# Performance work log

Hardware: AMD Instinct MI355X
Metric: run time of the kernel (lower is better)

The kernel has to match this reference:

```python
import jax, jax.numpy as jnp
import numpy as np

SOFTCLAMP = 50.0
CAUSAL_BLOCK = 256      # causal_block_size (tokens per time block)
NUM_SPECIAL = 8         # num_special_tokens
SPECIAL_SEQ = 2048      # block_size_per_special (defaults to kv seq len)
ROPE_BASE = 10000.0


def setup_inputs() -> dict:
    key = jax.random.key(0)
    kq, kk, kv = jax.random.split(key, 3)
    b, h, hk, s, d = 2, 16, 4, 2048, 64
    q = jax.random.normal(kq, (b, h, s, d), dtype=jnp.float32)
    k = jax.random.normal(kk, (b, hk, s, d), dtype=jnp.float32)
    v = jax.random.normal(kv, (b, hk, s, d), dtype=jnp.float32)
    # standard 1D rotary angles: [seq, dim_head]
    inv_freq = 1.0 / (ROPE_BASE ** (jnp.arange(0, d, 2, dtype=jnp.float32) / d))
    freqs = jnp.arange(s, dtype=jnp.float32)[:, None] * inv_freq[None, :]  # [s, d/2]
    rotations = jnp.concatenate((freqs, freqs), axis=-1)                   # [s, d]
    return {"q": q, "k": k, "v": v, "rotations": rotations}


def _apply_rotations(rotations, t):
    # t: [b, h, s, d]; rotations: [s, d] (broadcast over batch/heads)
    x1, x2 = jnp.split(t, 2, axis=-1)
    rotated_half = jnp.concatenate((-x2, x1), axis=-1)
    return t * jnp.cos(rotations) + rotated_half * jnp.sin(rotations)


def _forward(q, k, v, rotations):
    b, h, i, d = q.shape
    hk, j = k.shape[1], k.shape[2]
    scale = d ** -0.5
    q = _apply_rotations(rotations[:i], q)
    k = _apply_rotations(rotations[:j], k)
    g = h // hk  # GQA groups
    qg = q.reshape(b, hk, g, i, d)
    sim = jnp.einsum('bhgid,bhjd->bhgij', qg, k) * scale
    # softclamp score mod
    sim = jnp.tanh(sim / SOFTCLAMP) * SOFTCLAMP
    # special-token mask (faithful to source: compares raw q/k indices)
    qi = jnp.arange(i)[:, None]
    kj = jnp.arange(j)[None, :]
    special_start = SPECIAL_SEQ - NUM_SPECIAL
    q_is_special = qi >= special_start
    k_is_special = kj >= special_start
    special_mask = ~(~q_is_special & k_is_special)  # non-special q cannot see special k
    # block-causal mask: allowed when query block >= key block
    causal_allow = (qi // CAUSAL_BLOCK) >= (kj // CAUSAL_BLOCK)
    allow = special_mask & causal_allow  # [i, j], broadcasts over b,h,g
    mask_value = -jnp.finfo(sim.dtype).max
    sim = jnp.where(allow, sim, mask_value)
    attn = jax.nn.softmax(sim, axis=-1)
    out = jnp.einsum('bhgij,bhjd->bhgid', attn, v)
    return out.reshape(b, h, i, d)


def reference(q, k, v, rotations):
    return _forward(q, k, v, rotations)
```

## Files before the change

kernel.cpp:

```cpp
#include <hip/hip_runtime.h>
#include <stdint.h>

typedef unsigned short u16;
typedef short s16x8 __attribute__((ext_vector_type(8)));
typedef float f32x4 __attribute__((ext_vector_type(4)));

#define SQ 2048
#define DH 64
#define BM 128
#define BN 64
#define STR 72
#define SPECIAL_START 2040
#define NBH 32
#define NKV 8
#define NQP 16
#define NITEMS (NBH * NQP)
#define ATTN_GRID 448
#define K1F  0.18033688011112043f
#define KPAF 4.9244826e-9f
#define KPBF -6.406040185576019e-5f
#define KEF  36.067376022224085f

union U8 { s16x8 v; short e[8]; };
union F4 { f32x4 v; float e[4]; };

__device__ __forceinline__ u16 f2bf(float x) {
    uint32_t u = __float_as_uint(x);
    return (u16)((u + 0x7fffu + ((u >> 16) & 1u)) >> 16);
}
__device__ __forceinline__ uint32_t pkbf(float a, float b) {
    uint32_t r;
    asm("v_cvt_pk_bf16_f32 %0, %1, %2" : "=v"(r) : "v"(a), "v"(b));
    return r;
}
__device__ __forceinline__ float exp2hw(float x) {
    float r; asm("v_exp_f32 %0, %1" : "=v"(r) : "v"(x)); return r;
}
__device__ __forceinline__ float2 fsincos(float ang) {
    float r = ang * 0.15915494309189535f;
    r -= floorf(r);
    float s, c;
    asm("v_sin_f32 %0, %1" : "=v"(s) : "v"(r));
    asm("v_cos_f32 %0, %1" : "=v"(c) : "v"(r));
    return make_float2(s, c);
}

#define VTILES (NKV * 32)
#define RK (NKV * SQ)
#define KBLK (RK / 32)
__global__ __launch_bounds__(256)
void prep_kernel(const float* __restrict__ kg, const float* __restrict__ vg,
                 const float* __restrict__ rotg,
                 u16* __restrict__ kp, u16* __restrict__ vp,
                 uint32_t* __restrict__ cnt)
{
    const int tid = threadIdx.x;
    if (blockIdx.x == 0 && tid == 0) *cnt = 0u;
    if (blockIdx.x < VTILES) {
        __shared__ short Vls[64 * STR];
        const int tile = blockIdx.x;
        const float* src = vg + ((size_t)(tile >> 5) * SQ + (size_t)(tile & 31) * 64) * DH;
        {
            int kv = tid >> 2, c0 = (tid & 3) * 16;
            const float* s4 = src + (size_t)kv * DH + c0;
            float4 f0 = *(const float4*)(s4);
            float4 f1 = *(const float4*)(s4 + 4);
            float4 f2 = *(const float4*)(s4 + 8);
            float4 f3 = *(const float4*)(s4 + 12);
            uint4 w0 = make_uint4(pkbf(f0.x, f0.y), pkbf(f0.z, f0.w),
                                  pkbf(f1.x, f1.y), pkbf(f1.z, f1.w));
            uint4 w1 = make_uint4(pkbf(f2.x, f2.y), pkbf(f2.z, f2.w),
                                  pkbf(f3.x, f3.y), pkbf(f3.z, f3.w));
            *(uint4*)&Vls[kv * STR + c0]     = w0;
            *(uint4*)&Vls[kv * STR + c0 + 8] = w1;
        }
        __syncthreads();
        {
            int d = tid >> 2, c0 = (tid & 3) * 16;
            U8 o0, o1;
#pragma unroll
            for (int j = 0; j < 16; j++)
                (j < 8 ? o0 : o1).e[j & 7] = Vls[(c0 + j) * STR + d];
            u16* dst = vp + (((size_t)tile * 64 + d) << 6) + c0;
            *(s16x8*)dst       = o0.v;
            *(s16x8*)(dst + 8) = o1.v;
        }
    } else {
        int bx = blockIdx.x - VTILES;
        int r8 = tid >> 3, c0 = (tid & 7) * 4;
        int r = bx * 32 + r8;
        const int s = r & (SQ - 1);
        const float* src = kg + (size_t)r * DH;
        u16*         dst = kp + (size_t)r * DH;
        float4 a  = *(const float4*)(src + c0);
        float4 b  = *(const float4*)(src + c0 + 32);
        float4 rv = *(const float4*)(rotg + (size_t)s * DH + c0);
        float2 s0 = fsincos(rv.x), s1 = fsincos(rv.y),
               s2 = fsincos(rv.z), s3 = fsincos(rv.w);
        float lo0 = a.x * s0.y - b.x * s0.x, hi0 = b.x * s0.y + a.x * s0.x;
        float lo1 = a.y * s1.y - b.y * s1.x, hi1 = b.y * s1.y + a.y * s1.x;
        float lo2 = a.z * s2.y - b.z * s2.x, hi2 = b.z * s2.y + a.z * s2.x;
        float lo3 = a.w * s3.y - b.w * s3.x, hi3 = b.w * s3.y + a.w * s3.x;
        *(uint2*)(dst + c0)      = make_uint2(pkbf(lo0, lo1), pkbf(lo2, lo3));
        *(uint2*)(dst + c0 + 32) = make_uint2(pkbf(hi0, hi1), pkbf(hi2, hi3));
    }
}

__global__ __launch_bounds__(256, 3)
void attn_fast(const float* __restrict__ qg, const float* __restrict__ rotg,
               const u16* __restrict__ kp, const u16* __restrict__ vp,
               uint32_t* __restrict__ cnt, float* __restrict__ outg)
{
    const int tid = threadIdx.x;
    const int wv = tid >> 6, lane = tid & 63;
    const int l15 = lane & 15, quad = lane >> 4;
    const int swl = (l15 & 7) << 3;
    const int r4 = tid >> 2, c16 = (tid & 3) * 16;
    const int swr = (r4 & 7) << 3;

    __shared__ __align__(16) short Ks[2][BN * 64];
    __shared__ __align__(16) short Vt[2][DH * 64];
    __shared__ __align__(16) short Ps[BM * 64];
    __shared__ int s_w;

    for (;;) {
        __syncthreads();
        if (tid == 0) s_w = (int)atomicAdd(cnt, 1u);
        __syncthreads();
        const int w = s_w;
        if (w >= NITEMS) break;
        const int qp = (NQP - 1) - (w >> 5);
        const int u  = w & 31, bkv = u >> 2;
        const int bh = ((bkv >> 2) << 4) | ((bkv & 3) << 2) | (u & 3);
        const int nkt = ((qp >> 1) + 1) << 2;
        const int qrow0 = qp * BM + wv * 32;

        s16x8 qf[2][2];
#pragma unroll
        for (int nq = 0; nq < 2; nq++) {
            const int srow = qrow0 + nq * 16 + l15;
            const float* gq = qg + ((size_t)bh * SQ + srow) * DH + quad * 8;
            float a[8], b[8];
            *(float4*)&a[0] = *(const float4*)(gq);
            *(float4*)&a[4] = *(const float4*)(gq + 4);
            *(float4*)&b[0] = *(const float4*)(gq + 32);
            *(float4*)&b[4] = *(const float4*)(gq + 36);
            const float* rrow = rotg + (size_t)srow * DH + quad * 8;
            float lo[8], hi[8];
#pragma unroll
            for (int j = 0; j < 8; j++) {
                float2 sc = fsincos(rrow[j]);
                lo[j] = a[j] * sc.y - b[j] * sc.x;
                hi[j] = b[j] * sc.y + a[j] * sc.x;
            }
            U8 q0, q1;
#pragma unroll
            for (int j = 0; j < 4; j++) {
                ((uint32_t*)&q0.v)[j] = pkbf(lo[2 * j], lo[2 * j + 1]);
                ((uint32_t*)&q1.v)[j] = pkbf(hi[2 * j], hi[2 * j + 1]);
            }
            qf[nq][0] = q0.v;
            qf[nq][1] = q1.v;
        }

        const u16* kbase = kp + (size_t)bkv * (SQ * DH);
        const u16* vbase = vp + (size_t)bkv * (32 * 64 * 64);
        s16x8 kpr0, kpr1, vpr0, vpr1;
        auto pref = [&](int kt) {
            const u16* srck = kbase + (size_t)(kt * BN + r4) * DH + c16;
            kpr0 = *(const s16x8*)srck;
            kpr1 = *(const s16x8*)(srck + 8);
            const u16* srcv = vbase + ((size_t)kt << 12) + (r4 << 6) + c16;
            vpr0 = *(const s16x8*)srcv;
            vpr1 = *(const s16x8*)(srcv + 8);
        };
        pref(0);

        F4 oa[2][4];
#pragma unroll
        for (int nq = 0; nq < 2; nq++)
#pragma unroll
            for (int mb = 0; mb < 4; mb++) oa[nq][mb].v = (f32x4){0.f, 0.f, 0.f, 0.f};
        float lsum0 = 0.f, lsum1 = 0.f;
        short* prow0 = &Ps[(wv * 32 + l15) * 64];
        short* prow1 = &Ps[(wv * 32 + 16 + l15) * 64];

#pragma unroll 2
        for (int kt = 0; kt < nkt; kt++) {
            const int cb = kt & 1;
            *(s16x8*)&Ks[cb][r4 * 64 + (c16 ^ swr)]        = kpr0;
            *(s16x8*)&Ks[cb][r4 * 64 + ((c16 + 8) ^ swr)]  = kpr1;
            *(s16x8*)&Vt[cb][r4 * 64 + (c16 ^ swr)]        = vpr0;
            *(s16x8*)&Vt[cb][r4 * 64 + ((c16 + 8) ^ swr)]  = vpr1;
            if (kt + 1 < nkt) pref(kt + 1);
            __syncthreads();

            F4 sa[2][4];
            __builtin_amdgcn_s_setprio(1);
#pragma unroll
            for (int ks = 0; ks < 2; ks++)
#pragma unroll
                for (int mb = 0; mb < 4; mb++) {
                    s16x8 kf = *(const s16x8*)&Ks[cb][(mb * 16 + l15) * 64 + ((ks * 32 + quad * 8) ^ swl)];
                    sa[0][mb].v = __builtin_amdgcn_mfma_f32_16x16x32_bf16(
                        kf, qf[0][ks], ks ? sa[0][mb].v : (f32x4){0.f, 0.f, 0.f, 0.f}, 0, 0, 0);
                    sa[1][mb].v = __builtin_amdgcn_mfma_f32_16x16x32_bf16(
                        kf, qf[1][ks], ks ? sa[1][mb].v : (f32x4){0.f, 0.f, 0.f, 0.f}, 0, 0, 0);
                }
            __builtin_amdgcn_s_setprio(0);

            const int last = (kt == 31);
#pragma unroll
            for (int nq = 0; nq < 2; nq++) {
                const int qglob = qrow0 + nq * 16 + l15;
                short* prow = nq ? prow1 : prow0;
                float ls = 0.f;
#pragma unroll
                for (int mb = 0; mb < 4; mb++) {
                    F4 pa;
#pragma unroll
                    for (int c = 0; c < 4; c++) {
                        float t  = sa[nq][mb].e[c] * K1F;
                        float w2 = t * t;
                        float poly = fmaf(w2, fmaf(w2, KPAF, KPBF), 1.0f);
                        pa.e[c] = exp2hw(fmaf(t, poly, -KEF));
                    }
                    if (last && qglob < SPECIAL_START) {
#pragma unroll
                        for (int c = 0; c < 4; c++) {
                            int kvglob = kt * BN + mb * 16 + quad * 4 + c;
                            if (kvglob >= SPECIAL_START) pa.e[c] = 0.f;
                        }
                    }
                    ls += (pa.e[0] + pa.e[1]) + (pa.e[2] + pa.e[3]);
                    uint2 pw = make_uint2(pkbf(pa.e[0], pa.e[1]),
                                          pkbf(pa.e[2], pa.e[3]));
                    *(uint2*)&prow[(mb * 16 + quad * 4) ^ swl] = pw;
                }
                if (nq) lsum1 += ls; else lsum0 += ls;
            }

            __builtin_amdgcn_s_setprio(1);
#pragma unroll
            for (int ks = 0; ks < 2; ks++) {
                s16x8 pf0 = *(const s16x8*)&prow0[(ks * 32 + quad * 8) ^ swl];
                s16x8 pf1 = *(const s16x8*)&prow1[(ks * 32 + quad * 8) ^ swl];
#pragma unroll
                for (int mb = 0; mb < 4; mb++) {
                    s16x8 vf = *(const s16x8*)&Vt[cb][(mb * 16 + l15) * 64 + ((ks * 32 + quad * 8) ^ swl)];
                    oa[0][mb].v = __builtin_amdgcn_mfma_f32_16x16x32_bf16(vf, pf0, oa[0][mb].v, 0, 0, 0);
                    oa[1][mb].v = __builtin_amdgcn_mfma_f32_16x16x32_bf16(vf, pf1, oa[1][mb].v, 0, 0, 0);
                }
            }
            __builtin_amdgcn_s_setprio(0);
        }

        lsum0 += __shfl_xor(lsum0, 16, 64);
        lsum0 += __shfl_xor(lsum0, 32, 64);
        lsum1 += __shfl_xor(lsum1, 16, 64);
        lsum1 += __shfl_xor(lsum1, 32, 64);

#pragma unroll
        for (int nq = 0; nq < 2; nq++) {
            float rl = 1.0f / (nq ? lsum1 : lsum0);
            int qrow = qrow0 + nq * 16 + l15;
            float* orow = outg + ((size_t)bh * SQ + qrow) * DH;
#pragma unroll
            for (int mb = 0; mb < 4; mb++) {
                int d0 = mb * 16 + quad * 4;
                *(float4*)(orow + d0) = make_float4(oa[nq][mb].e[0] * rl, oa[nq][mb].e[1] * rl,
                                                    oa[nq][mb].e[2] * rl, oa[nq][mb].e[3] * rl);
            }
        }
    }
}

__global__ __launch_bounds__(256, 4)
void attn_fallback(const float* __restrict__ qg, const float* __restrict__ kg,
                   const float* __restrict__ vg, const float* __restrict__ rotg,
                   float* __restrict__ outg)
{
    const int x  = blockIdx.x;
    const int qt = (x & 1) ? (31 - (x >> 1)) : (x >> 1);
    const int bh = blockIdx.y;
    const int bb = bh >> 4, hh = bh & 15;
    const int bkv = bb * 4 + (hh >> 2);
    const int qs = qt * 64;

    const int tid = threadIdx.x;
    const int wv = tid >> 6, lane = tid & 63;
    const int l15 = lane & 15, quad = lane >> 4;
    const int swl = (l15 & 7) << 3;

    __shared__ __align__(16) short QPs[64 * 64];
    __shared__ __align__(16) short Ks[2][BN * 64];
    __shared__ __align__(16) short Vt[2][DH * 64];

    const size_t kvbase = ((size_t)bkv * SQ) * DH;
    const int nkt = (qt / 4 + 1) * 4;
    const int qglob = qs + wv * 16 + l15;

    {
        int rr = tid >> 2, c0 = (tid & 3) * 8;
        int srow = qs + rr;
        const float* gq = qg + ((size_t)bh * SQ + srow) * DH;
        float a[8], b[8];
        *(float4*)&a[0] = *(const float4*)(gq + c0);
        *(float4*)&a[4] = *(const float4*)(gq + c0 + 4);
        *(float4*)&b[0] = *(const float4*)(gq + c0 + 32);
        *(float4*)&b[4] = *(const float4*)(gq + c0 + 36);
        U8 o0, o1;
#pragma unroll
        for (int j = 0; j < 8; j++) {
            float2 sc = fsincos(rotg[(size_t)srow * DH + c0 + j]);
            o0.e[j] = (short)f2bf(a[j] * sc.y - b[j] * sc.x);
            o1.e[j] = (short)f2bf(b[j] * sc.y + a[j] * sc.x);
        }
        int sw2 = (rr & 7) << 3;
        *(s16x8*)&QPs[rr * 64 + (c0 ^ sw2)]        = o0.v;
        *(s16x8*)&QPs[rr * 64 + ((c0 + 32) ^ sw2)] = o1.v;
    }
    __syncthreads();

    s16x8 qf[2];
#pragma unroll
    for (int ks = 0; ks < 2; ks++)
        qf[ks] = *(const s16x8*)&QPs[(wv * 16 + l15) * 64 + ((ks * 32 + quad * 8) ^ swl)];

    F4 oa[4];
#pragma unroll
    for (int mb = 0; mb < 4; mb++) oa[mb].v = (f32x4){0.f, 0.f, 0.f, 0.f};
    float lsum = 0.f;

    for (int kt = 0; kt < nkt; kt++) {
        const int cb = kt & 1;
        {
            int rr = tid >> 2, c0 = (tid & 3) * 8;
            int srow = kt * BN + rr;
            const float* gk = kg + kvbase + (size_t)srow * DH;
            float a[8], b[8];
            *(float4*)&a[0] = *(const float4*)(gk + c0);
            *(float4*)&a[4] = *(const float4*)(gk + c0 + 4);
            *(float4*)&b[0] = *(const float4*)(gk + c0 + 32);
            *(float4*)&b[4] = *(const float4*)(gk + c0 + 36);
            U8 o0, o1;
#pragma unroll
            for (int j = 0; j < 8; j++) {
                float2 sc = fsincos(rotg[(size_t)(srow & (SQ - 1)) * DH + c0 + j]);
                o0.e[j] = (short)f2bf(a[j] * sc.y - b[j] * sc.x);
                o1.e[j] = (short)f2bf(b[j] * sc.y + a[j] * sc.x);
            }
            int sw2 = (rr & 7) << 3;
            *(s16x8*)&Ks[cb][rr * 64 + (c0 ^ sw2)]        = o0.v;
            *(s16x8*)&Ks[cb][rr * 64 + ((c0 + 32) ^ sw2)] = o1.v;
        }
        {
            int rr = tid >> 2, c0 = (tid & 3) * 16;
            const float* gv = vg + kvbase + (size_t)(kt * BN + rr) * DH;
            float vv[16];
#pragma unroll
            for (int t = 0; t < 4; t++)
                *(float4*)&vv[t * 4] = *(const float4*)(gv + c0 + t * 4);
#pragma unroll
            for (int j = 0; j < 16; j++) {
                int d = c0 + j;
                Vt[cb][d * 64 + (rr ^ ((d & 7) << 3))] = (short)f2bf(vv[j]);
            }
        }
        __syncthreads();

        F4 sa[4];
#pragma unroll
        for (int mb = 0; mb < 4; mb++) sa[mb].v = (f32x4){0.f, 0.f, 0.f, 0.f};
#pragma unroll
        for (int ks = 0; ks < 2; ks++)
#pragma unroll
            for (int mb = 0; mb < 4; mb++) {
                s16x8 kf = *(const s16x8*)&Ks[cb][(mb * 16 + l15) * 64 + ((ks * 32 + quad * 8) ^ swl)];
                sa[mb].v = __builtin_amdgcn_mfma_f32_16x16x32_bf16(kf, qf[ks], sa[mb].v, 0, 0, 0);
            }

        F4 pa[4];
#pragma unroll
        for (int mb = 0; mb < 4; mb++)
#pragma unroll
            for (int c = 0; c < 4; c++) {
                float t  = sa[mb].e[c] * K1F;
                float w2 = t * t;
                float poly = fmaf(w2, fmaf(w2, KPAF, KPBF), 1.0f);
                pa[mb].e[c] = exp2hw(fmaf(t, poly, -KEF));
            }
        if (kt == 31 && qglob < SPECIAL_START) {
#pragma unroll
            for (int mb = 0; mb < 4; mb++)
#pragma unroll
                for (int c = 0; c < 4; c++) {
                    int kvglob = kt * BN + mb * 16 + quad * 4 + c;
                    if (kvglob >= SPECIAL_START) pa[mb].e[c] = 0.f;
                }
        }
        short* prow = &QPs[(wv * 16 + l15) * 64];
#pragma unroll
        for (int mb = 0; mb < 4; mb++) {
            lsum += (pa[mb].e[0] + pa[mb].e[1]) + (pa[mb].e[2] + pa[mb].e[3]);
            uint2 pw = make_uint2(pkbf(pa[mb].e[0], pa[mb].e[1]),
                                  pkbf(pa[mb].e[2], pa[mb].e[3]));
            *(uint2*)&prow[(mb * 16 + quad * 4) ^ swl] = pw;
        }
#pragma unroll
        for (int ks = 0; ks < 2; ks++) {
            s16x8 pf = *(const s16x8*)&prow[(ks * 32 + quad * 8) ^ swl];
#pragma unroll
            for (int mb = 0; mb < 4; mb++) {
                s16x8 vf = *(const s16x8*)&Vt[cb][(mb * 16 + l15) * 64 + ((ks * 32 + quad * 8) ^ swl)];
                oa[mb].v = __builtin_amdgcn_mfma_f32_16x16x32_bf16(vf, pf, oa[mb].v, 0, 0, 0);
            }
        }
        __syncthreads();
    }

    lsum += __shfl_xor(lsum, 16, 64);
    lsum += __shfl_xor(lsum, 32, 64);

    float rl = 1.0f / lsum;
    int qrow = qs + wv * 16 + l15;
    float* orow = outg + ((size_t)bh * SQ + qrow) * DH;
#pragma unroll
    for (int mb = 0; mb < 4; mb++) {
        int d0 = mb * 16 + quad * 4;
        *(float4*)(orow + d0) = make_float4(oa[mb].e[0] * rl, oa[mb].e[1] * rl,
                                            oa[mb].e[2] * rl, oa[mb].e[3] * rl);
    }
}

extern "C" void kernel_launch(void* const* d_in, const int* in_sizes, int n_in,
                              void* d_out, int out_size, void* d_ws, size_t ws_size,
                              hipStream_t stream) {
    const float* q   = (const float*)d_in[0];
    const float* k   = (const float*)d_in[1];
    const float* v   = (const float*)d_in[2];
    const float* rot = (const float*)d_in[3];
    float* out = (float*)d_out;

    char* w = (char*)d_ws;
    const size_t k_bytes = (size_t)NKV * SQ * DH * sizeof(u16);
    const size_t v_bytes = k_bytes;
    u16* kp = (u16*)w;
    u16* vp = (u16*)(w + k_bytes);
    uint32_t* cnt = (uint32_t*)(w + k_bytes + v_bytes);

    if (ws_size >= k_bytes + v_bytes + sizeof(uint32_t)) {
        hipLaunchKernelGGL(prep_kernel, dim3(VTILES + KBLK), dim3(256), 0, stream,
                           k, v, rot, kp, vp, cnt);
        hipLaunchKernelGGL(attn_fast, dim3(ATTN_GRID), dim3(256), 0, stream,
                           q, rot, kp, vp, cnt, out);
    } else {
        hipLaunchKernelGGL(attn_fallback, dim3(32, NBH), dim3(256), 0, stream,
                           q, k, v, rot, out);
    }
}
```

Measured before the change: 135.8 us.

## Split each query tile's KV range across two wave groups per block

The attention block grows to 512 threads, split into two groups of four waves. Each group processes half of the query tile's key/value tiles using its own LDS staging. The second group writes its partial output and row sums to shared memory, and the first group adds them in before normalising and storing. The goal is to halve per-work-item latency and cut tail imbalance from causal work skew in the persistent scheduler. In exchange, K/V double buffering is dropped, an extra barrier is added per tile, a combine step is added, and the grid size changes.

```diff
diff --git a/kernel.cpp b/kernel.cpp
--- a/kernel.cpp
+++ b/kernel.cpp
@@ -15,7 +15,7 @@
 #define NKV 8
 #define NQP 16
 #define NITEMS (NBH * NQP)
-#define ATTN_GRID 448
+#define ATTN_GRID 480
 #define K1F  0.18033688011112043f
 #define KPAF 4.9244826e-9f
 #define KPBF -6.406040185576019e-5f
@@ -106,7 +106,7 @@
     }
 }
 
-__global__ __launch_bounds__(256, 3)
+__global__ __launch_bounds__(512, 4)
 void attn_fast(const float* __restrict__ qg, const float* __restrict__ rotg,
                const u16* __restrict__ kp, const u16* __restrict__ vp,
                uint32_t* __restrict__ cnt, float* __restrict__ outg)
@@ -114,14 +114,19 @@
     const int tid = threadIdx.x;
     const int wv = tid >> 6, lane = tid & 63;
     const int l15 = lane & 15, quad = lane >> 4;
+    const int grp = wv >> 2, wl = wv & 3;
+    const int tl = tid & 255;
+    const int r4 = tl >> 2, c16 = (tl & 3) * 16;
+    const int swr = (r4 & 7) << 3;
     const int swl = (l15 & 7) << 3;
-    const int r4 = tid >> 2, c16 = (tid & 3) * 16;
-    const int swr = (r4 & 7) << 3;
-
-    __shared__ __align__(16) short Ks[2][BN * 64];
-    __shared__ __align__(16) short Vt[2][DH * 64];
-    __shared__ __align__(16) short Ps[BM * 64];
+
+    __shared__ __align__(16) short SM[32768];
     __shared__ int s_w;
+    short* Ksg  = SM + grp * 4096;
+    short* Vtg  = SM + 8192 + grp * 4096;
+    short* Psg  = SM + 16384 + grp * 8192;
+    float* comb  = (float*)SM;
+    float* lsumB = (float*)(SM + 16384);
 
     for (;;) {
         __syncthreads();
@@ -133,35 +138,9 @@
         const int u  = w & 31, bkv = u >> 2;
         const int bh = ((bkv >> 2) << 4) | ((bkv & 3) << 2) | (u & 3);
         const int nkt = ((qp >> 1) + 1) << 2;
-        const int qrow0 = qp * BM + wv * 32;
-
-        s16x8 qf[2][2];
-#pragma unroll
-        for (int nq = 0; nq < 2; nq++) {
-            const int srow = qrow0 + nq * 16 + l15;
-            const float* gq = qg + ((size_t)bh * SQ + srow) * DH + quad * 8;
-            float a[8], b[8];
-            *(float4*)&a[0] = *(const float4*)(gq);
-            *(float4*)&a[4] = *(const float4*)(gq + 4);
-            *(float4*)&b[0] = *(const float4*)(gq + 32);
-            *(float4*)&b[4] = *(const float4*)(gq + 36);
-            const float* rrow = rotg + (size_t)srow * DH + quad * 8;
-            float lo[8], hi[8];
-#pragma unroll
-            for (int j = 0; j < 8; j++) {
-                float2 sc = fsincos(rrow[j]);
-                lo[j] = a[j] * sc.y - b[j] * sc.x;
-                hi[j] = b[j] * sc.y + a[j] * sc.x;
-            }
-            U8 q0, q1;
-#pragma unroll
-            for (int j = 0; j < 4; j++) {
-                ((uint32_t*)&q0.v)[j] = pkbf(lo[2 * j], lo[2 * j + 1]);
-                ((uint32_t*)&q1.v)[j] = pkbf(hi[2 * j], hi[2 * j + 1]);
-            }
-            qf[nq][0] = q0.v;
-            qf[nq][1] = q1.v;
-        }
+        const int h   = nkt >> 1;
+        const int kt0 = grp ? h : 0;
+        const int qrow0 = qp * BM + wl * 32;
 
         const u16* kbase = kp + (size_t)bkv * (SQ * DH);
         const u16* vbase = vp + (size_t)bkv * (32 * 64 * 64);
@@ -174,7 +153,35 @@
             vpr0 = *(const s16x8*)srcv;
             vpr1 = *(const s16x8*)(srcv + 8);
         };
-        pref(0);
+        pref(kt0);
+
+        s16x8 qf[2][2];
+#pragma unroll
+        for (int nq = 0; nq < 2; nq++) {
+            const int srow = qrow0 + nq * 16 + l15;
+            const float* gq = qg + ((size_t)bh * SQ + srow) * DH + quad * 8;
+            float a[8], b[8];
+            *(float4*)&a[0] = *(const float4*)(gq);
+            *(float4*)&a[4] = *(const float4*)(gq + 4);
+            *(float4*)&b[0] = *(const float4*)(gq + 32);
+            *(float4*)&b[4] = *(const float4*)(gq + 36);
+            const float* rrow = rotg + (size_t)srow * DH + quad * 8;
+            float lo[8], hi[8];
+#pragma unroll
+            for (int j = 0; j < 8; j++) {
+                float2 sc = fsincos(rrow[j]);
+                lo[j] = a[j] * sc.y - b[j] * sc.x;
+                hi[j] = b[j] * sc.y + a[j] * sc.x;
+            }
+            U8 q0, q1;
+#pragma unroll
+            for (int j = 0; j < 4; j++) {
+                ((uint32_t*)&q0.v)[j] = pkbf(lo[2 * j], lo[2 * j + 1]);
+                ((uint32_t*)&q1.v)[j] = pkbf(hi[2 * j], hi[2 * j + 1]);
+            }
+            qf[nq][0] = q0.v;
+            qf[nq][1] = q1.v;
+        }
 
         F4 oa[2][4];
 #pragma unroll
@@ -182,17 +189,16 @@
 #pragma unroll
             for (int mb = 0; mb < 4; mb++) oa[nq][mb].v = (f32x4){0.f, 0.f, 0.f, 0.f};
         float lsum0 = 0.f, lsum1 = 0.f;
-        short* prow0 = &Ps[(wv * 32 + l15) * 64];
-        short* prow1 = &Ps[(wv * 32 + 16 + l15) * 64];
-
-#pragma unroll 2
-        for (int kt = 0; kt < nkt; kt++) {
-            const int cb = kt & 1;
-            *(s16x8*)&Ks[cb][r4 * 64 + (c16 ^ swr)]        = kpr0;
-            *(s16x8*)&Ks[cb][r4 * 64 + ((c16 + 8) ^ swr)]  = kpr1;
-            *(s16x8*)&Vt[cb][r4 * 64 + (c16 ^ swr)]        = vpr0;
-            *(s16x8*)&Vt[cb][r4 * 64 + ((c16 + 8) ^ swr)]  = vpr1;
-            if (kt + 1 < nkt) pref(kt + 1);
+        short* prow0 = &Psg[(wl * 32 + l15) * 64];
+        short* prow1 = &Psg[(wl * 32 + 16 + l15) * 64];
+
+        for (int i = 0; i < h; i++) {
+            const int kt = kt0 + i;
+            *(s16x8*)&Ksg[r4 * 64 + (c16 ^ swr)]       = kpr0;
+            *(s16x8*)&Ksg[r4 * 64 + ((c16 + 8) ^ swr)] = kpr1;
+            *(s16x8*)&Vtg[r4 * 64 + (c16 ^ swr)]       = vpr0;
+            *(s16x8*)&Vtg[r4 * 64 + ((c16 + 8) ^ swr)] = vpr1;
+            if (i + 1 < h) pref(kt + 1);
             __syncthreads();
 
             F4 sa[2][4];
@@ -201,7 +207,7 @@
             for (int ks = 0; ks < 2; ks++)
 #pragma unroll
                 for (int mb = 0; mb < 4; mb++) {
-                    s16x8 kf = *(const s16x8*)&Ks[cb][(mb * 16 + l15) * 64 + ((ks * 32 + quad * 8) ^ swl)];
+                    s16x8 kf = *(const s16x8*)&Ksg[(mb * 16 + l15) * 64 + ((ks * 32 + quad * 8) ^ swl)];
                     sa[0][mb].v = __builtin_amdgcn_mfma_f32_16x16x32_bf16(
                         kf, qf[0][ks], ks ? sa[0][mb].v : (f32x4){0.f, 0.f, 0.f, 0.f}, 0, 0, 0);
                     sa[1][mb].v = __builtin_amdgcn_mfma_f32_16x16x32_bf16(
@@ -247,12 +253,13 @@
                 s16x8 pf1 = *(const s16x8*)&prow1[(ks * 32 + quad * 8) ^ swl];
 #pragma unroll
                 for (int mb = 0; mb < 4; mb++) {
-                    s16x8 vf = *(const s16x8*)&Vt[cb][(mb * 16 + l15) * 64 + ((ks * 32 + quad * 8) ^ swl)];
+                    s16x8 vf = *(const s16x8*)&Vtg[(mb * 16 + l15) * 64 + ((ks * 32 + quad * 8) ^ swl)];
                     oa[0][mb].v = __builtin_amdgcn_mfma_f32_16x16x32_bf16(vf, pf0, oa[0][mb].v, 0, 0, 0);
                     oa[1][mb].v = __builtin_amdgcn_mfma_f32_16x16x32_bf16(vf, pf1, oa[1][mb].v, 0, 0, 0);
                 }
             }
             __builtin_amdgcn_s_setprio(0);
+            __syncthreads();
         }
 
         lsum0 += __shfl_xor(lsum0, 16, 64);
@@ -260,16 +267,34 @@
         lsum1 += __shfl_xor(lsum1, 16, 64);
         lsum1 += __shfl_xor(lsum1, 32, 64);
 
-#pragma unroll
-        for (int nq = 0; nq < 2; nq++) {
-            float rl = 1.0f / (nq ? lsum1 : lsum0);
-            int qrow = qrow0 + nq * 16 + l15;
-            float* orow = outg + ((size_t)bh * SQ + qrow) * DH;
-#pragma unroll
-            for (int mb = 0; mb < 4; mb++) {
-                int d0 = mb * 16 + quad * 4;
-                *(float4*)(orow + d0) = make_float4(oa[nq][mb].e[0] * rl, oa[nq][mb].e[1] * rl,
-                                                    oa[nq][mb].e[2] * rl, oa[nq][mb].e[3] * rl);
+        if (grp) {
+#pragma unroll
+            for (int nq = 0; nq < 2; nq++) {
+                const int row = wl * 32 + nq * 16 + l15;
+#pragma unroll
+                for (int mb = 0; mb < 4; mb++)
+                    *(float4*)&comb[row * 64 + mb * 16 + quad * 4] =
+                        make_float4(oa[nq][mb].e[0], oa[nq][mb].e[1],
+                                    oa[nq][mb].e[2], oa[nq][mb].e[3]);
+                if (quad == 0) lsumB[row] = nq ? lsum1 : lsum0;
+            }
+        }
+        __syncthreads();
+        if (!grp) {
+#pragma unroll
+            for (int nq = 0; nq < 2; nq++) {
+                const int row = wl * 32 + nq * 16 + l15;
+                const float rl = 1.0f / ((nq ? lsum1 : lsum0) + lsumB[row]);
+                float* orow = outg + ((size_t)bh * SQ + qp * BM + row) * DH;
+#pragma unroll
+                for (int mb = 0; mb < 4; mb++) {
+                    const int d0 = mb * 16 + quad * 4;
+                    float4 cb = *(float4*)&comb[row * 64 + d0];
+                    *(float4*)(orow + d0) = make_float4((oa[nq][mb].e[0] + cb.x) * rl,
+                                                        (oa[nq][mb].e[1] + cb.y) * rl,
+                                                        (oa[nq][mb].e[2] + cb.z) * rl,
+                                                        (oa[nq][mb].e[3] + cb.w) * rl);
+                }
             }
         }
     }
@@ -452,7 +477,7 @@
     if (ws_size >= k_bytes + v_bytes + sizeof(uint32_t)) {
         hipLaunchKernelGGL(prep_kernel, dim3(VTILES + KBLK), dim3(256), 0, stream,
                            k, v, rot, kp, vp, cnt);
-        hipLaunchKernelGGL(attn_fast, dim3(ATTN_GRID), dim3(256), 0, stream,
+        hipLaunchKernelGGL(attn_fast, dim3(ATTN_GRID), dim3(512), 0, stream,
                            q, rot, kp, vp, cnt, out);
     } else {
         hipLaunchKernelGGL(attn_fallback, dim3(32, NBH), dim3(256), 0, stream,
```

New measurement: 135.7 us. About the same (-0.1%).

## Make attention waves independent, loading K/V fragments directly from global memory

Applied to the files above, without the earlier changes.

Each wave now takes its own 32-row query work item from the atomic queue instead of a 4-wave block sharing one 128-row tile. The shared-memory staging of K and V and the block barriers are removed, and each wave loads MFMA fragments for K and V straight from global memory, prefetching the next tile after each MFMA phase. The P buffer becomes per-wave with padded stride, the row sums accumulate as vectors, and the grid grows to 768 blocks. The cost is no K/V reuse across the waves of a block, so global and L2 traffic rises, plus more atomics.

```diff
diff --git a/kernel.cpp b/kernel.cpp
--- a/kernel.cpp
+++ b/kernel.cpp
@@ -7,15 +7,14 @@
 
 #define SQ 2048
 #define DH 64
-#define BM 128
 #define BN 64
 #define STR 72
+#define PSTR 72
 #define SPECIAL_START 2040
 #define NBH 32
 #define NKV 8
-#define NQP 16
-#define NITEMS (NBH * NQP)
-#define ATTN_GRID 448
+#define NITEMS 2048
+#define ATTN_BLOCKS 768
 #define K1F  0.18033688011112043f
 #define KPAF 4.9244826e-9f
 #define KPBF -6.406040185576019e-5f
@@ -106,39 +105,58 @@
     }
 }
 
-__global__ __launch_bounds__(256, 3)
+__global__ __launch_bounds__(256)
+__attribute__((amdgpu_waves_per_eu(3, 3)))
 void attn_fast(const float* __restrict__ qg, const float* __restrict__ rotg,
                const u16* __restrict__ kp, const u16* __restrict__ vp,
                uint32_t* __restrict__ cnt, float* __restrict__ outg)
 {
-    const int tid = threadIdx.x;
-    const int wv = tid >> 6, lane = tid & 63;
+    const int lane = threadIdx.x & 63;
+    const int wv   = threadIdx.x >> 6;
     const int l15 = lane & 15, quad = lane >> 4;
-    const int swl = (l15 & 7) << 3;
-    const int r4 = tid >> 2, c16 = (tid & 3) * 16;
-    const int swr = (r4 & 7) << 3;
-
-    __shared__ __align__(16) short Ks[2][BN * 64];
-    __shared__ __align__(16) short Vt[2][DH * 64];
-    __shared__ __align__(16) short Ps[BM * 64];
-    __shared__ int s_w;
+
+    __shared__ __align__(16) short Ps[4][32 * PSTR];
+    short* prow0 = &Ps[wv][l15 * PSTR];
+    short* prow1 = &Ps[wv][(16 + l15) * PSTR];
 
     for (;;) {
-        __syncthreads();
-        if (tid == 0) s_w = (int)atomicAdd(cnt, 1u);
-        __syncthreads();
-        const int w = s_w;
+        int w = 0;
+        if (lane == 0) w = (int)atomicAdd(cnt, 1u);
+        w = __shfl(w, 0, 64);
         if (w >= NITEMS) break;
-        const int qp = (NQP - 1) - (w >> 5);
-        const int u  = w & 31, bkv = u >> 2;
-        const int bh = ((bkv >> 2) << 4) | ((bkv & 3) << 2) | (u & 3);
-        const int nkt = ((qp >> 1) + 1) << 2;
-        const int qrow0 = qp * BM + wv * 32;
+        const int idx = 63 - (w >> 5);
+        const int u   = w & 31, bkv = u >> 2;
+        const int bh  = ((bkv >> 2) << 4) | ((bkv & 3) << 2) | (u & 3);
+        const int qs  = idx * 32;
+        const int nkt = ((idx >> 3) + 1) << 2;
+
+        const u16* kptr = kp + (size_t)bkv * (SQ * DH) + l15 * DH + quad * 8;
+        const u16* vptr = vp + (size_t)bkv * (SQ * DH) + l15 * DH + quad * 8;
+
+        s16x8 kf0[4], kf1[4], vf0[4], vf1[4];
+        auto loadK = [&](int kt) {
+            const u16* p = kptr + ((size_t)kt << 12);
+#pragma unroll
+            for (int mb = 0; mb < 4; mb++) {
+                kf0[mb] = *(const s16x8*)(p + mb * 1024);
+                kf1[mb] = *(const s16x8*)(p + mb * 1024 + 32);
+            }
+        };
+        auto loadV = [&](int kt) {
+            const u16* p = vptr + ((size_t)kt << 12);
+#pragma unroll
+            for (int mb = 0; mb < 4; mb++) {
+                vf0[mb] = *(const s16x8*)(p + mb * 1024);
+                vf1[mb] = *(const s16x8*)(p + mb * 1024 + 32);
+            }
+        };
+        loadK(0);
+        loadV(0);
 
         s16x8 qf[2][2];
 #pragma unroll
         for (int nq = 0; nq < 2; nq++) {
-            const int srow = qrow0 + nq * 16 + l15;
+            const int srow = qs + nq * 16 + l15;
             const float* gq = qg + ((size_t)bh * SQ + srow) * DH + quad * 8;
             float a[8], b[8];
             *(float4*)&a[0] = *(const float4*)(gq);
@@ -163,68 +181,52 @@
             qf[nq][1] = q1.v;
         }
 
-        const u16* kbase = kp + (size_t)bkv * (SQ * DH);
-        const u16* vbase = vp + (size_t)bkv * (32 * 64 * 64);
-        s16x8 kpr0, kpr1, vpr0, vpr1;
-        auto pref = [&](int kt) {
-            const u16* srck = kbase + (size_t)(kt * BN + r4) * DH + c16;
-            kpr0 = *(const s16x8*)srck;
-            kpr1 = *(const s16x8*)(srck + 8);
-            const u16* srcv = vbase + ((size_t)kt << 12) + (r4 << 6) + c16;
-            vpr0 = *(const s16x8*)srcv;
-            vpr1 = *(const s16x8*)(srcv + 8);
-        };
-        pref(0);
-
-        F4 oa[2][4];
-#pragma unroll
-        for (int nq = 0; nq < 2; nq++)
-#pragma unroll
-            for (int mb = 0; mb < 4; mb++) oa[nq][mb].v = (f32x4){0.f, 0.f, 0.f, 0.f};
-        float lsum0 = 0.f, lsum1 = 0.f;
-        short* prow0 = &Ps[(wv * 32 + l15) * 64];
-        short* prow1 = &Ps[(wv * 32 + 16 + l15) * 64];
-
-#pragma unroll 2
+        F4 oa0[4], oa1[4], lsa0, lsa1;
+#pragma unroll
+        for (int mb = 0; mb < 4; mb++) {
+            oa0[mb].v = (f32x4){0.f, 0.f, 0.f, 0.f};
+            oa1[mb].v = (f32x4){0.f, 0.f, 0.f, 0.f};
+        }
+        lsa0.v = (f32x4){0.f, 0.f, 0.f, 0.f};
+        lsa1.v = (f32x4){0.f, 0.f, 0.f, 0.f};
+
         for (int kt = 0; kt < nkt; kt++) {
-            const int cb = kt & 1;
-            *(s16x8*)&Ks[cb][r4 * 64 + (c16 ^ swr)]        = kpr0;
-            *(s16x8*)&Ks[cb][r4 * 64 + ((c16 + 8) ^ swr)]  = kpr1;
-            *(s16x8*)&Vt[cb][r4 * 64 + (c16 ^ swr)]        = vpr0;
-            *(s16x8*)&Vt[cb][r4 * 64 + ((c16 + 8) ^ swr)]  = vpr1;
-            if (kt + 1 < nkt) pref(kt + 1);
-            __syncthreads();
-
-            F4 sa[2][4];
+            F4 sa0[4], sa1[4];
             __builtin_amdgcn_s_setprio(1);
 #pragma unroll
-            for (int ks = 0; ks < 2; ks++)
+            for (int mb = 0; mb < 4; mb++) {
+                sa0[mb].v = __builtin_amdgcn_mfma_f32_16x16x32_bf16(
+                    kf0[mb], qf[0][0], (f32x4){0.f, 0.f, 0.f, 0.f}, 0, 0, 0);
+                sa1[mb].v = __builtin_amdgcn_mfma_f32_16x16x32_bf16(
+                    kf0[mb], qf[1][0], (f32x4){0.f, 0.f, 0.f, 0.f}, 0, 0, 0);
+            }
+#pragma unroll
+            for (int mb = 0; mb < 4; mb++) {
+                sa0[mb].v = __builtin_amdgcn_mfma_f32_16x16x32_bf16(
+                    kf1[mb], qf[0][1], sa0[mb].v, 0, 0, 0);
+                sa1[mb].v = __builtin_amdgcn_mfma_f32_16x16x32_bf16(
+                    kf1[mb], qf[1][1], sa1[mb].v, 0, 0, 0);
+            }
+            __builtin_amdgcn_s_setprio(0);
+            if (kt + 1 < nkt) loadK(kt + 1);
+
+            const int last = (kt == 31);
+#pragma unroll
+            for (int nq = 0; nq < 2; nq++) {
+                const int qglob = qs + nq * 16 + l15;
+                short* prow = nq ? prow1 : prow0;
 #pragma unroll
                 for (int mb = 0; mb < 4; mb++) {
-                    s16x8 kf = *(const s16x8*)&Ks[cb][(mb * 16 + l15) * 64 + ((ks * 32 + quad * 8) ^ swl)];
-                    sa[0][mb].v = __builtin_amdgcn_mfma_f32_16x16x32_bf16(
-                        kf, qf[0][ks], ks ? sa[0][mb].v : (f32x4){0.f, 0.f, 0.f, 0.f}, 0, 0, 0);
-                    sa[1][mb].v = __builtin_amdgcn_mfma_f32_16x16x32_bf16(
-                        kf, qf[1][ks], ks ? sa[1][mb].v : (f32x4){0.f, 0.f, 0.f, 0.f}, 0, 0, 0);
-                }
-            __builtin_amdgcn_s_setprio(0);
-
-            const int last = (kt == 31);
-#pragma unroll
-            for (int nq = 0; nq < 2; nq++) {
-                const int qglob = qrow0 + nq * 16 + l15;
-                short* prow = nq ? prow1 : prow0;
-                float ls = 0.f;
-#pragma unroll
-                for (int mb = 0; mb < 4; mb++) {
-                    F4 pa;
-#pragma unroll
-                    for (int c = 0; c < 4; c++) {
-                        float t  = sa[nq][mb].e[c] * K1F;
-                        float w2 = t * t;
-                        float poly = fmaf(w2, fmaf(w2, KPAF, KPBF), 1.0f);
-                        pa.e[c] = exp2hw(fmaf(t, poly, -KEF));
-                    }
+                    F4 t, w2, py, pa;
+                    t.v  = (nq ? sa1[mb].v : sa0[mb].v) * K1F;
+                    w2.v = t.v * t.v;
+                    py.v = w2.v * KPAF + KPBF;
+                    py.v = w2.v * py.v + 1.0f;
+                    t.v  = t.v * py.v - KEF;
+                    pa.e[0] = exp2hw(t.e[0]);
+                    pa.e[1] = exp2hw(t.e[1]);
+                    pa.e[2] = exp2hw(t.e[2]);
+                    pa.e[3] = exp2hw(t.e[3]);
                     if (last && qglob < SPECIAL_START) {
 #pragma unroll
                         for (int c = 0; c < 4; c++) {
@@ -232,29 +234,34 @@
                             if (kvglob >= SPECIAL_START) pa.e[c] = 0.f;
                         }
                     }
-                    ls += (pa.e[0] + pa.e[1]) + (pa.e[2] + pa.e[3]);
+                    if (nq) lsa1.v = lsa1.v + pa.v; else lsa0.v = lsa0.v + pa.v;
                     uint2 pw = make_uint2(pkbf(pa.e[0], pa.e[1]),
                                           pkbf(pa.e[2], pa.e[3]));
-                    *(uint2*)&prow[(mb * 16 + quad * 4) ^ swl] = pw;
+                    *(uint2*)&prow[mb * 16 + quad * 4] = pw;
                 }
-                if (nq) lsum1 += ls; else lsum0 += ls;
-            }
-
+            }
+
+            s16x8 pf00 = *(const s16x8*)&prow0[quad * 8];
+            s16x8 pf01 = *(const s16x8*)&prow0[32 + quad * 8];
+            s16x8 pf10 = *(const s16x8*)&prow1[quad * 8];
+            s16x8 pf11 = *(const s16x8*)&prow1[32 + quad * 8];
             __builtin_amdgcn_s_setprio(1);
 #pragma unroll
-            for (int ks = 0; ks < 2; ks++) {
-                s16x8 pf0 = *(const s16x8*)&prow0[(ks * 32 + quad * 8) ^ swl];
-                s16x8 pf1 = *(const s16x8*)&prow1[(ks * 32 + quad * 8) ^ swl];
-#pragma unroll
-                for (int mb = 0; mb < 4; mb++) {
-                    s16x8 vf = *(const s16x8*)&Vt[cb][(mb * 16 + l15) * 64 + ((ks * 32 + quad * 8) ^ swl)];
-                    oa[0][mb].v = __builtin_amdgcn_mfma_f32_16x16x32_bf16(vf, pf0, oa[0][mb].v, 0, 0, 0);
-                    oa[1][mb].v = __builtin_amdgcn_mfma_f32_16x16x32_bf16(vf, pf1, oa[1][mb].v, 0, 0, 0);
-                }
+            for (int mb = 0; mb < 4; mb++) {
+                oa0[mb].v = __builtin_amdgcn_mfma_f32_16x16x32_bf16(vf0[mb], pf00, oa0[mb].v, 0, 0, 0);
+                oa1[mb].v = __builtin_amdgcn_mfma_f32_16x16x32_bf16(vf0[mb], pf10, oa1[mb].v, 0, 0, 0);
+            }
+#pragma unroll
+            for (int mb = 0; mb < 4; mb++) {
+                oa0[mb].v = __builtin_amdgcn_mfma_f32_16x16x32_bf16(vf1[mb], pf01, oa0[mb].v, 0, 0, 0);
+                oa1[mb].v = __builtin_amdgcn_mfma_f32_16x16x32_bf16(vf1[mb], pf11, oa1[mb].v, 0, 0, 0);
             }
             __builtin_amdgcn_s_setprio(0);
-        }
-
+            if (kt + 1 < nkt) loadV(kt + 1);
+        }
+
+        float lsum0 = (lsa0.e[0] + lsa0.e[1]) + (lsa0.e[2] + lsa0.e[3]);
+        float lsum1 = (lsa1.e[0] + lsa1.e[1]) + (lsa1.e[2] + lsa1.e[3]);
         lsum0 += __shfl_xor(lsum0, 16, 64);
         lsum0 += __shfl_xor(lsum0, 32, 64);
         lsum1 += __shfl_xor(lsum1, 16, 64);
@@ -262,14 +269,15 @@
 
 #pragma unroll
         for (int nq = 0; nq < 2; nq++) {
-            float rl = 1.0f / (nq ? lsum1 : lsum0);
-            int qrow = qrow0 + nq * 16 + l15;
+            const float rl = 1.0f / (nq ? lsum1 : lsum0);
+            const int qrow = qs + nq * 16 + l15;
             float* orow = outg + ((size_t)bh * SQ + qrow) * DH;
 #pragma unroll
             for (int mb = 0; mb < 4; mb++) {
-                int d0 = mb * 16 + quad * 4;
-                *(float4*)(orow + d0) = make_float4(oa[nq][mb].e[0] * rl, oa[nq][mb].e[1] * rl,
-                                                    oa[nq][mb].e[2] * rl, oa[nq][mb].e[3] * rl);
+                const int d0 = mb * 16 + quad * 4;
+                const F4& o = nq ? oa1[mb] : oa0[mb];
+                *(float4*)(orow + d0) = make_float4(o.e[0] * rl, o.e[1] * rl,
+                                                    o.e[2] * rl, o.e[3] * rl);
             }
         }
     }
@@ -452,7 +460,7 @@
     if (ws_size >= k_bytes + v_bytes + sizeof(uint32_t)) {
         hipLaunchKernelGGL(prep_kernel, dim3(VTILES + KBLK), dim3(256), 0, stream,
                            k, v, rot, kp, vp, cnt);
-        hipLaunchKernelGGL(attn_fast, dim3(ATTN_GRID), dim3(256), 0, stream,
+        hipLaunchKernelGGL(attn_fast, dim3(ATTN_BLOCKS), dim3(256), 0, stream,
                            q, rot, kp, vp, cnt, out);
     } else {
         hipLaunchKernelGGL(attn_fallback, dim3(32, NBH), dim3(256), 0, stream,
```

Measured after the change: 215.1 us. 1.58x slower.

## Stage K/V tiles with direct global-to-LDS loads and restructure the pipeline

Applied to the files above, without the earlier changes.

K and V tiles now go straight from global memory into LDS through global_load_lds, replacing the register prefetch and the explicit LDS stores. The barrier moves to the end of each iteration, and the swizzle is folded into the global read offsets. The grid size and occupancy hints change, the exp polynomial is vectorized, and the row sums are kept as vector accumulators. The aim is to cut VGPR pressure and LDS store instructions, at the risk of a synchronization hazard if the async LDS writes are not fully waited on before use.

```diff
diff --git a/kernel.cpp b/kernel.cpp
--- a/kernel.cpp
+++ b/kernel.cpp
@@ -7,7 +7,6 @@
 
 #define SQ 2048
 #define DH 64
-#define BM 128
 #define BN 64
 #define STR 72
 #define SPECIAL_START 2040
@@ -15,7 +14,7 @@
 #define NKV 8
 #define NQP 16
 #define NITEMS (NBH * NQP)
-#define ATTN_GRID 448
+#define ATTN_GRID 512
 #define K1F  0.18033688011112043f
 #define KPAF 4.9244826e-9f
 #define KPBF -6.406040185576019e-5f
@@ -43,6 +42,11 @@
     asm("v_sin_f32 %0, %1" : "=v"(s) : "v"(r));
     asm("v_cos_f32 %0, %1" : "=v"(c) : "v"(r));
     return make_float2(s, c);
+}
+__device__ __forceinline__ void gl_lds16(const void* g, void* l) {
+    __builtin_amdgcn_global_load_lds(
+        (const __attribute__((address_space(1))) uint32_t*)g,
+        (__attribute__((address_space(3))) uint32_t*)l, 16, 0, 0);
 }
 
 #define VTILES (NKV * 32)
@@ -106,7 +110,8 @@
     }
 }
 
-__global__ __launch_bounds__(256, 3)
+__global__ __launch_bounds__(256)
+__attribute__((amdgpu_waves_per_eu(3, 4)))
 void attn_fast(const float* __restrict__ qg, const float* __restrict__ rotg,
                const u16* __restrict__ kp, const u16* __restrict__ vp,
                uint32_t* __restrict__ cnt, float* __restrict__ outg)
@@ -115,13 +120,20 @@
     const int wv = tid >> 6, lane = tid & 63;
     const int l15 = lane & 15, quad = lane >> 4;
     const int swl = (l15 & 7) << 3;
-    const int r4 = tid >> 2, c16 = (tid & 3) * 16;
-    const int swr = (r4 & 7) << 3;
-
-    __shared__ __align__(16) short Ks[2][BN * 64];
-    __shared__ __align__(16) short Vt[2][DH * 64];
-    __shared__ __align__(16) short Ps[BM * 64];
+
+    __shared__ __align__(16) u16 Ks[2][4096];
+    __shared__ __align__(16) u16 Vt[2][4096];
+    __shared__ __align__(16) short Ps[128 * 64];
     __shared__ int s_w;
+
+    const int gcol = (((lane & 7) ^ (lane >> 3)) << 3);
+    const int goff0 = ((wv * 16 + (lane >> 3)) << 6) + gcol;
+    const int goff1 = goff0 + (8 << 6);
+    const int lds0 = (wv * 2) * 512;
+    const int lds1 = lds0 + 512;
+
+    short* prow0 = &Ps[(wv * 32 + l15) * 64];
+    short* prow1 = &Ps[(wv * 32 + 16 + l15) * 64];
 
     for (;;) {
         __syncthreads();
@@ -132,8 +144,20 @@
         const int qp = (NQP - 1) - (w >> 5);
         const int u  = w & 31, bkv = u >> 2;
         const int bh = ((bkv >> 2) << 4) | ((bkv & 3) << 2) | (u & 3);
-        const int nkt = ((qp >> 1) + 1) << 2;
-        const int qrow0 = qp * BM + wv * 32;
+        const int nkt = (((qp >> 1) + 1)) << 2;
+        const int qrow0 = qp * 128 + wv * 32;
+
+        const u16* kbase = kp + (size_t)bkv * (SQ * DH);
+        const u16* vbase = vp + (size_t)bkv * (SQ * DH);
+        auto stage = [&](int kt, int cb) {
+            const u16* tk = kbase + ((size_t)kt << 12);
+            const u16* tv = vbase + ((size_t)kt << 12);
+            gl_lds16(tk + goff0, &Ks[cb][lds0]);
+            gl_lds16(tk + goff1, &Ks[cb][lds1]);
+            gl_lds16(tv + goff0, &Vt[cb][lds0]);
+            gl_lds16(tv + goff1, &Vt[cb][lds1]);
+        };
+        stage(0, 0);
 
         s16x8 qf[2][2];
 #pragma unroll
@@ -163,37 +187,20 @@
             qf[nq][1] = q1.v;
         }
 
-        const u16* kbase = kp + (size_t)bkv * (SQ * DH);
-        const u16* vbase = vp + (size_t)bkv * (32 * 64 * 64);
-        s16x8 kpr0, kpr1, vpr0, vpr1;
-        auto pref = [&](int kt) {
-            const u16* srck = kbase + (size_t)(kt * BN + r4) * DH + c16;
-            kpr0 = *(const s16x8*)srck;
-            kpr1 = *(const s16x8*)(srck + 8);
-            const u16* srcv = vbase + ((size_t)kt << 12) + (r4 << 6) + c16;
-            vpr0 = *(const s16x8*)srcv;
-            vpr1 = *(const s16x8*)(srcv + 8);
-        };
-        pref(0);
-
         F4 oa[2][4];
 #pragma unroll
         for (int nq = 0; nq < 2; nq++)
 #pragma unroll
             for (int mb = 0; mb < 4; mb++) oa[nq][mb].v = (f32x4){0.f, 0.f, 0.f, 0.f};
-        float lsum0 = 0.f, lsum1 = 0.f;
-        short* prow0 = &Ps[(wv * 32 + l15) * 64];
-        short* prow1 = &Ps[(wv * 32 + 16 + l15) * 64];
-
-#pragma unroll 2
+        F4 lsa0, lsa1;
+        lsa0.v = (f32x4){0.f, 0.f, 0.f, 0.f};
+        lsa1.v = (f32x4){0.f, 0.f, 0.f, 0.f};
+
+        __syncthreads();
+        int cb = 0;
+
         for (int kt = 0; kt < nkt; kt++) {
-            const int cb = kt & 1;
-            *(s16x8*)&Ks[cb][r4 * 64 + (c16 ^ swr)]        = kpr0;
-            *(s16x8*)&Ks[cb][r4 * 64 + ((c16 + 8) ^ swr)]  = kpr1;
-            *(s16x8*)&Vt[cb][r4 * 64 + (c16 ^ swr)]        = vpr0;
-            *(s16x8*)&Vt[cb][r4 * 64 + ((c16 + 8) ^ swr)]  = vpr1;
-            if (kt + 1 < nkt) pref(kt + 1);
-            __syncthreads();
+            if (kt + 1 < nkt) stage(kt + 1, cb ^ 1);
 
             F4 sa[2][4];
             __builtin_amdgcn_s_setprio(1);
@@ -214,17 +221,18 @@
             for (int nq = 0; nq < 2; nq++) {
                 const int qglob = qrow0 + nq * 16 + l15;
                 short* prow = nq ? prow1 : prow0;
-                float ls = 0.f;
 #pragma unroll
                 for (int mb = 0; mb < 4; mb++) {
-                    F4 pa;
-#pragma unroll
-                    for (int c = 0; c < 4; c++) {
-                        float t  = sa[nq][mb].e[c] * K1F;
-                        float w2 = t * t;
-                        float poly = fmaf(w2, fmaf(w2, KPAF, KPBF), 1.0f);
-                        pa.e[c] = exp2hw(fmaf(t, poly, -KEF));
-                    }
+                    F4 t, w2, py, pa;
+                    t.v  = sa[nq][mb].v * K1F;
+                    w2.v = t.v * t.v;
+                    py.v = w2.v * KPAF + KPBF;
+                    py.v = w2.v * py.v + 1.0f;
+                    t.v  = t.v * py.v - KEF;
+                    pa.e[0] = exp2hw(t.e[0]);
+                    pa.e[1] = exp2hw(t.e[1]);
+                    pa.e[2] = exp2hw(t.e[2]);
+                    pa.e[3] = exp2hw(t.e[3]);
                     if (last && qglob < SPECIAL_START) {
 #pragma unroll
                         for (int c = 0; c < 4; c++) {
@@ -232,29 +240,38 @@
                             if (kvglob >= SPECIAL_START) pa.e[c] = 0.f;
                         }
                     }
-                    ls += (pa.e[0] + pa.e[1]) + (pa.e[2] + pa.e[3]);
+                    if (nq) lsa1.v = lsa1.v + pa.v; else lsa0.v = lsa0.v + pa.v;
                     uint2 pw = make_uint2(pkbf(pa.e[0], pa.e[1]),
                                           pkbf(pa.e[2], pa.e[3]));
                     *(uint2*)&prow[(mb * 16 + quad * 4) ^ swl] = pw;
                 }
-                if (nq) lsum1 += ls; else lsum0 += ls;
-            }
-
+            }
+
+            s16x8 pf00 = *(const s16x8*)&prow0[(quad * 8) ^ swl];
+            s16x8 pf01 = *(const s16x8*)&prow0[(32 + quad * 8) ^ swl];
+            s16x8 pf10 = *(const s16x8*)&prow1[(quad * 8) ^ swl];
+            s16x8 pf11 = *(const s16x8*)&prow1[(32 + quad * 8) ^ swl];
             __builtin_amdgcn_s_setprio(1);
 #pragma unroll
-            for (int ks = 0; ks < 2; ks++) {
-                s16x8 pf0 = *(const s16x8*)&prow0[(ks * 32 + quad * 8) ^ swl];
-                s16x8 pf1 = *(const s16x8*)&prow1[(ks * 32 + quad * 8) ^ swl];
-#pragma unroll
-                for (int mb = 0; mb < 4; mb++) {
-                    s16x8 vf = *(const s16x8*)&Vt[cb][(mb * 16 + l15) * 64 + ((ks * 32 + quad * 8) ^ swl)];
-                    oa[0][mb].v = __builtin_amdgcn_mfma_f32_16x16x32_bf16(vf, pf0, oa[0][mb].v, 0, 0, 0);
-                    oa[1][mb].v = __builtin_amdgcn_mfma_f32_16x16x32_bf16(vf, pf1, oa[1][mb].v, 0, 0, 0);
-                }
+            for (int mb = 0; mb < 4; mb++) {
+                s16x8 vf = *(const s16x8*)&Vt[cb][(mb * 16 + l15) * 64 + ((quad * 8) ^ swl)];
+                oa[0][mb].v = __builtin_amdgcn_mfma_f32_16x16x32_bf16(vf, pf00, oa[0][mb].v, 0, 0, 0);
+                oa[1][mb].v = __builtin_amdgcn_mfma_f32_16x16x32_bf16(vf, pf10, oa[1][mb].v, 0, 0, 0);
+            }
+#pragma unroll
+            for (int mb = 0; mb < 4; mb++) {
+                s16x8 vf = *(const s16x8*)&Vt[cb][(mb * 16 + l15) * 64 + ((32 + quad * 8) ^ swl)];
+                oa[0][mb].v = __builtin_amdgcn_mfma_f32_16x16x32_bf16(vf, pf01, oa[0][mb].v, 0, 0, 0);
+                oa[1][mb].v = __builtin_amdgcn_mfma_f32_16x16x32_bf16(vf, pf11, oa[1][mb].v, 0, 0, 0);
             }
             __builtin_amdgcn_s_setprio(0);
-        }
-
+
+            __syncthreads();
+            cb ^= 1;
+        }
+
+        float lsum0 = (lsa0.e[0] + lsa0.e[1]) + (lsa0.e[2] + lsa0.e[3]);
+        float lsum1 = (lsa1.e[0] + lsa1.e[1]) + (lsa1.e[2] + lsa1.e[3]);
         lsum0 += __shfl_xor(lsum0, 16, 64);
         lsum0 += __shfl_xor(lsum0, 32, 64);
         lsum1 += __shfl_xor(lsum1, 16, 64);
@@ -262,14 +279,15 @@
 
 #pragma unroll
         for (int nq = 0; nq < 2; nq++) {
-            float rl = 1.0f / (nq ? lsum1 : lsum0);
-            int qrow = qrow0 + nq * 16 + l15;
+            const float rl = 1.0f / (nq ? lsum1 : lsum0);
+            const int qrow = qrow0 + nq * 16 + l15;
             float* orow = outg + ((size_t)bh * SQ + qrow) * DH;
 #pragma unroll
             for (int mb = 0; mb < 4; mb++) {
-                int d0 = mb * 16 + quad * 4;
-                *(float4*)(orow + d0) = make_float4(oa[nq][mb].e[0] * rl, oa[nq][mb].e[1] * rl,
-                                                    oa[nq][mb].e[2] * rl, oa[nq][mb].e[3] * rl);
+                const int d0 = mb * 16 + quad * 4;
+                const F4& o = oa[nq][mb];
+                *(float4*)(orow + d0) = make_float4(o.e[0] * rl, o.e[1] * rl,
+                                                    o.e[2] * rl, o.e[3] * rl);
             }
         }
     }
```

Result: faster. 129.7 us (-4.5%).
